# Optimization experiments

Measured on AMD Instinct MI355X. Metric: run time of the kernel, lower is better.

Reference implementation:

```python
import jax, jax.numpy as jnp
import numpy as np

TAU = 2.0
V_TH = 1.0
SG_ALPHA = 4.0  # spikingjelly surrogate.Sigmoid default

@jax.custom_vjp
def spike_fn(u):
    # heaviside(u) with sigmoid surrogate gradient; u = v - v_threshold
    return (u >= 0.0).astype(u.dtype)

def _spike_fwd(u):
    return spike_fn(u), u

def _spike_bwd(u, g):
    s = jax.nn.sigmoid(SG_ALPHA * u)
    return (g * SG_ALPHA * s * (1.0 - s),)

spike_fn.defvjp(_spike_fwd, _spike_bwd)

def lif_scan(h):
    # h: [T, B, D] input currents; multi-step LIF with hard reset to 0,
    # decay_input=True: v = v + (h - v) / tau
    def step(v, h_t):
        v = v + (h_t - v) / TAU
        s = spike_fn(v - V_TH)
        v = v * (1.0 - jax.lax.stop_gradient(s))  # detach_reset=True, v_reset=0
        return v, s
    v0 = jnp.zeros_like(h[0])
    _, spikes = jax.lax.scan(step, v0, h)
    return spikes  # [T, B, D]

def setup_inputs() -> dict:
    key = jax.random.key(0)
    k_x, k_w1, k_b1, k_w2, k_b2 = jax.random.split(key, 5)
    T, B, D, C = 32, 512, 1024, 1000
    lim1 = 1.0 / np.sqrt(D)
    return {
        "x": jax.random.normal(k_x, (T, B, D), dtype=jnp.float32),
        "W1": jax.random.uniform(k_w1, (D, D), jnp.float32, -lim1, lim1),
        "b1": jax.random.uniform(k_b1, (D,), jnp.float32, -lim1, lim1),
        "W2": jax.random.uniform(k_w2, (C, D), jnp.float32, -lim1, lim1),
        "b2": jax.random.uniform(k_b2, (C,), jnp.float32, -lim1, lim1),
    }

def reference(x, W1, b1, W2, b2):
    # linear_1: [T,B,D] @ [D,D]^T + b1
    h = jnp.einsum('tbd,ed->tbe', x, W1) + b1
    s = lif_scan(h)                               # [T,B,D] spikes in {0,1}
    y = jnp.einsum('tbd,cd->tbc', s, W2) + b2     # [T,B,C]
    y = y.mean(axis=0)                            # [B,C]
    return jax.nn.log_softmax(y, axis=1)
```

## Files before the change

kernel.cpp:

```cpp
#include <hip/hip_runtime.h>
#include <math.h>

#define T_STEPS 32
#define B_SZ    512
#define D_SZ    1024
#define C_SZ    1000
#define KZ      8
#define HP      132

typedef __bf16 bf16x8 __attribute__((ext_vector_type(8)));
typedef float  f32x4  __attribute__((ext_vector_type(4)));

__device__ __forceinline__ unsigned short f2bf(float f) {
    unsigned u = __float_as_uint(f);
    unsigned r = u + 0x7FFFu + ((u >> 16) & 1u);
    return (unsigned short)(r >> 16);
}
__device__ __forceinline__ float bf2f(unsigned short b) {
    return __uint_as_float(((unsigned)b) << 16);
}

__device__ __forceinline__ void async_copy16(const void* g, void* l) {
    __builtin_amdgcn_global_load_lds(
        (const __attribute__((address_space(1))) unsigned int*)g,
        (__attribute__((address_space(3))) unsigned int*)l,
        16, 0, 0);
}

__device__ __forceinline__ bf16x8 cvt8(const float4 u, const float4 v) {
    bf16x8 r;
    r[0] = (__bf16)u.x; r[1] = (__bf16)u.y; r[2] = (__bf16)u.z; r[3] = (__bf16)u.w;
    r[4] = (__bf16)v.x; r[5] = (__bf16)v.y; r[6] = (__bf16)v.z; r[7] = (__bf16)v.w;
    return r;
}

#define NW14  262144
#define NW24  256000
#define NWTOT (NW14 + NW24)

__global__ __launch_bounds__(256) void cast_w_k(
    const float* __restrict__ W1, unsigned short* __restrict__ W1_bf,
    const float* __restrict__ W2, unsigned short* __restrict__ W2_bf)
{
    const int idx = blockIdx.x * 256 + threadIdx.x;
    const float4* s; ushort4* d; int j;
    if (idx < NW14) { s = (const float4*)W1; d = (ushort4*)W1_bf; j = idx; }
    else            { s = (const float4*)W2; d = (ushort4*)W2_bf; j = idx - NW14; }
    const float4 v = s[j];
    ushort4 o;
    o.x = f2bf(v.x); o.y = f2bf(v.y); o.z = f2bf(v.z); o.w = f2bf(v.w);
    d[j] = o;
}

__global__ __launch_bounds__(256) void gemm1_scan_k(
    const float* __restrict__ X, const unsigned short* __restrict__ Bm,
    const float* __restrict__ bias, unsigned short* __restrict__ cnt)
{
    __shared__ __align__(16) unsigned short smem[128 * HP];
    unsigned short* As = smem;
    unsigned short* Bs = smem + 8192;

    const int tid  = threadIdx.x;
    const int wave = tid >> 6;
    const int lane = tid & 63;
    const int lm   = lane & 15;
    const int quad = lane >> 4;
    const int wm   = (wave >> 1) * 64;
    const int wn   = (wave & 1) * 64;

    const int f  = blockIdx.x;
    const int yb = f & 127;
    const int xb = f >> 7;
    const int b0 = yb * 4;
    const int n0 = xb * 128;

    f32x4 acc[4][4];
    #pragma unroll
    for (int i = 0; i < 4; ++i)
        #pragma unroll
        for (int j = 0; j < 4; ++j)
            acc[i][j] = (f32x4){0.f, 0.f, 0.f, 0.f};

    int srow[4], sgq[4];
    size_t arowoff[4];
    unsigned ldsoffB[4];
    #pragma unroll
    for (int p = 0; p < 4; ++p) {
        const int s = p * 256 + tid;
        const int rho = s >> 3;
        srow[p] = rho;
        sgq[p]  = (s & 7) ^ (rho & 7);
        arowoff[p] = (size_t)((rho >> 2) * 512 + b0 + (rho & 3)) * D_SZ;
        ldsoffB[p] = (unsigned)(p * 256 + wave * 64) * 16u;
    }
    const int fq0 = quad ^ (lm & 7);

    for (int k0 = 0; k0 < D_SZ; k0 += 64) {
        #pragma unroll
        for (int p = 0; p < 4; ++p)
            async_copy16(Bm + (size_t)(n0 + srow[p]) * D_SZ + k0 + sgq[p] * 8,
                         (char*)Bs + ldsoffB[p]);
        #pragma unroll
        for (int p = 0; p < 4; ++p) {
            const float* src = X + arowoff[p] + k0 + sgq[p] * 8;
            const float4 u = *(const float4*)(src);
            const float4 v = *(const float4*)(src + 4);
            ((bf16x8*)As)[p * 256 + tid] = cvt8(u, v);
        }
        __syncthreads();

        #pragma unroll
        for (int kk = 0; kk < 2; ++kk) {
            const int fqk = fq0 ^ (kk * 4);
            bf16x8 af[4], bfr[4];
            #pragma unroll
            for (int i = 0; i < 4; ++i) {
                af[i]  = ((const bf16x8*)As)[(wm + i * 16 + lm) * 8 + fqk];
                bfr[i] = ((const bf16x8*)Bs)[(wn + i * 16 + lm) * 8 + fqk];
            }
            #pragma unroll
            for (int mi = 0; mi < 4; ++mi)
                #pragma unroll
                for (int ni = 0; ni < 4; ++ni)
                    acc[mi][ni] = __builtin_amdgcn_mfma_f32_16x16x32_bf16(
                        af[mi], bfr[ni], acc[mi][ni], 0, 0, 0);
        }
        __syncthreads();
    }

    #pragma unroll
    for (int ni = 0; ni < 4; ++ni) {
        const int nn = wn + ni * 16 + lm;
        const float bv = bias[n0 + nn];
        #pragma unroll
        for (int mi = 0; mi < 4; ++mi) {
            const f32x4 v = acc[mi][ni];
            #pragma unroll
            for (int r = 0; r < 4; ++r)
                smem[(wm + mi * 16 + quad * 4 + r) * HP + nn] = f2bf(v[r] + bv);
        }
    }
    __syncthreads();

    {
        const unsigned* smemU = (const unsigned*)smem;
        const int bb = tid >> 6;
        const int c2 = tid & 63;
        float v0 = 0.f, cv0 = 0.f, v1 = 0.f, cv1 = 0.f;
        #pragma unroll
        for (int t = 0; t < T_STEPS; ++t) {
            const unsigned u = smemU[(t * 4 + bb) * (HP / 2) + c2];
            const float h0 = bf2f((unsigned short)(u & 0xFFFFu));
            const float h1 = bf2f((unsigned short)(u >> 16));
            v0 = 0.5f * (v0 + h0);
            const float s0 = (v0 >= 1.0f) ? 1.0f : 0.0f;
            cv0 += s0; v0 *= (1.0f - s0);
            v1 = 0.5f * (v1 + h1);
            const float s1 = (v1 >= 1.0f) ? 1.0f : 0.0f;
            cv1 += s1; v1 *= (1.0f - s1);
        }
        ushort2 o;
        o.x = f2bf(cv0); o.y = f2bf(cv1);
        *(ushort2*)&cnt[(size_t)(b0 + bb) * D_SZ + n0 + 2 * c2] = o;
    }
}

__global__ __launch_bounds__(256) void gemm2_splitk_k(
    const unsigned short* __restrict__ A, const unsigned short* __restrict__ Bm,
    float* __restrict__ partial)
{
    __shared__ __align__(16) unsigned short As[128 * 32];
    __shared__ __align__(16) unsigned short Bs[128 * 32];

    const int tid  = threadIdx.x;
    const int wave = tid >> 6;
    const int lane = tid & 63;
    const int lm   = lane & 15;
    const int quad = lane >> 4;
    const int wm   = (wave >> 1) * 64;
    const int wn   = (wave & 1) * 64;
    const int n0   = blockIdx.x * 128;
    const int m0   = blockIdx.y * 128;
    const int kz   = blockIdx.z;

    f32x4 acc[4][4];
    #pragma unroll
    for (int i = 0; i < 4; ++i)
        #pragma unroll
        for (int j = 0; j < 4; ++j)
            acc[i][j] = (f32x4){0.f, 0.f, 0.f, 0.f};

    int srow[2], sgq[2];
    unsigned ldsoff[2];
    #pragma unroll
    for (int p = 0; p < 2; ++p) {
        const int s = p * 256 + tid;
        srow[p] = s >> 2;
        sgq[p]  = (s & 3) ^ ((srow[p] >> 1) & 3);
        ldsoff[p] = (unsigned)(p * 256 + wave * 64) * 16u;
    }
    const int fq = quad ^ ((lm >> 1) & 3);

    const int kbeg = kz * (D_SZ / KZ);
    for (int k0 = kbeg; k0 < kbeg + D_SZ / KZ; k0 += 32) {
        #pragma unroll
        for (int p = 0; p < 2; ++p) {
            async_copy16(A + (size_t)(m0 + srow[p]) * D_SZ + k0 + sgq[p] * 8,
                         (char*)As + ldsoff[p]);
            int brow = n0 + srow[p];
            if (brow > C_SZ - 1) brow = C_SZ - 1;
            async_copy16(Bm + (size_t)brow * D_SZ + k0 + sgq[p] * 8,
                         (char*)Bs + ldsoff[p]);
        }
        __syncthreads();

        bf16x8 af[4], bfr[4];
        #pragma unroll
        for (int i = 0; i < 4; ++i) {
            af[i]  = ((const bf16x8*)As)[(wm + i * 16 + lm) * 4 + fq];
            bfr[i] = ((const bf16x8*)Bs)[(wn + i * 16 + lm) * 4 + fq];
        }
        #pragma unroll
        for (int mi = 0; mi < 4; ++mi)
            #pragma unroll
            for (int ni = 0; ni < 4; ++ni)
                acc[mi][ni] = __builtin_amdgcn_mfma_f32_16x16x32_bf16(
                    af[mi], bfr[ni], acc[mi][ni], 0, 0, 0);
        __syncthreads();
    }

    #pragma unroll
    for (int ni = 0; ni < 4; ++ni) {
        const int nn = n0 + wn + ni * 16 + lm;
        if (nn >= C_SZ) continue;
        #pragma unroll
        for (int mi = 0; mi < 4; ++mi) {
            const f32x4 v = acc[mi][ni];
            #pragma unroll
            for (int r = 0; r < 4; ++r) {
                const int mm = m0 + wm + mi * 16 + quad * 4 + r;
                partial[((size_t)kz * B_SZ + mm) * C_SZ + nn] = v[r];
            }
        }
    }
}

__global__ __launch_bounds__(256) void reduce_lsm_k(
    const float* __restrict__ partial, const float* __restrict__ b2,
    float* __restrict__ out)
{
    __shared__ float red_max[4];
    __shared__ float red_sum[4];

    const int b   = blockIdx.x;
    const int tid = threadIdx.x;

    float vals[4];
    float m = -1e30f;
    #pragma unroll
    for (int k = 0; k < 4; ++k) {
        const int c = tid + k * 256;
        if (c < C_SZ) {
            float s = 0.f;
            #pragma unroll
            for (int z = 0; z < KZ; ++z)
                s += partial[((size_t)z * B_SZ + b) * C_SZ + c];
            vals[k] = s * (1.0f / (float)T_STEPS) + b2[c];
        } else {
            vals[k] = -1e30f;
        }
        m = fmaxf(m, vals[k]);
    }
    #pragma unroll
    for (int off = 32; off > 0; off >>= 1)
        m = fmaxf(m, __shfl_down(m, off, 64));
    const int wave = tid >> 6;
    const int lane = tid & 63;
    if (lane == 0) red_max[wave] = m;
    __syncthreads();
    m = fmaxf(fmaxf(red_max[0], red_max[1]), fmaxf(red_max[2], red_max[3]));

    float s = 0.f;
    #pragma unroll
    for (int k = 0; k < 4; ++k) {
        const int c = tid + k * 256;
        if (c < C_SZ) s += __expf(vals[k] - m);
    }
    #pragma unroll
    for (int off = 32; off > 0; off >>= 1)
        s += __shfl_down(s, off, 64);
    if (lane == 0) red_sum[wave] = s;
    __syncthreads();
    s = red_sum[0] + red_sum[1] + red_sum[2] + red_sum[3];

    const float lse = m + logf(s);
    #pragma unroll
    for (int k = 0; k < 4; ++k) {
        const int c = tid + k * 256;
        if (c < C_SZ) out[(size_t)b * C_SZ + c] = vals[k] - lse;
    }
}

extern "C" void kernel_launch(void* const* d_in, const int* in_sizes, int n_in,
                              void* d_out, int out_size, void* d_ws, size_t ws_size,
                              hipStream_t stream)
{
    const float* x  = (const float*)d_in[0];
    const float* W1 = (const float*)d_in[1];
    const float* b1 = (const float*)d_in[2];
    const float* W2 = (const float*)d_in[3];
    const float* b2 = (const float*)d_in[4];
    float* out = (float*)d_out;

    char* ws = (char*)d_ws;
    unsigned short* W1_bf   = (unsigned short*)(ws);
    unsigned short* W2_bf   = (unsigned short*)(ws + 2097152);
    unsigned short* cnt_bf  = (unsigned short*)(ws + 4145152);
    float*          partial = (float*)(ws + 5193728);

    cast_w_k<<<NWTOT / 256, 256, 0, stream>>>(W1, W1_bf, W2, W2_bf);

    gemm1_scan_k<<<(B_SZ / 4) * (D_SZ / 128), 256, 0, stream>>>(
        x, W1_bf, b1, cnt_bf);

    {
        dim3 grid((C_SZ + 127) / 128, B_SZ / 128, KZ);
        gemm2_splitk_k<<<grid, 256, 0, stream>>>(cnt_bf, W2_bf, partial);
    }

    reduce_lsm_k<<<B_SZ, 256, 0, stream>>>(partial, b2, out);
}
```

Measured before the change: 167.5 us.

## Double-buffer GEMM1 LDS tiles with register prefetch and swizzled block order

Converts the GEMM1 main loop into a double-buffered pipeline: the next A tile is prefetched into registers and the next B tile is staged asynchronously into a second LDS buffer while MFMAs run on the current buffer. This drops one barrier per k-step. Compute sections are wrapped in s_setprio so the MFMA waves get issue priority. The block index mapping is also remapped into 8x8 groups for better L2 reuse of X and W1 tiles. In exchange, LDS grows to 64KB and register use rises, which may cut occupancy.

```diff
diff --git a/kernel.cpp b/kernel.cpp
--- a/kernel.cpp
+++ b/kernel.cpp
@@ -56,9 +56,7 @@
     const float* __restrict__ X, const unsigned short* __restrict__ Bm,
     const float* __restrict__ bias, unsigned short* __restrict__ cnt)
 {
-    __shared__ __align__(16) unsigned short smem[128 * HP];
-    unsigned short* As = smem;
-    unsigned short* Bs = smem + 8192;
+    __shared__ __align__(16) unsigned short smem[32768];
 
     const int tid  = threadIdx.x;
     const int wave = tid >> 6;
@@ -69,8 +67,11 @@
     const int wn   = (wave & 1) * 64;
 
     const int f  = blockIdx.x;
-    const int yb = f & 127;
-    const int xb = f >> 7;
+    const int rr = f >> 9;
+    const int cc = f & 7;
+    const int ss = (f >> 3) & 63;
+    const int xb = ss & 7;
+    const int yb = rr * 64 + (ss >> 3) * 8 + cc;
     const int b0 = yb * 4;
     const int n0 = xb * 128;
 
@@ -95,38 +96,85 @@
     }
     const int fq0 = quad ^ (lm & 7);
 
-    for (int k0 = 0; k0 < D_SZ; k0 += 64) {
-        #pragma unroll
-        for (int p = 0; p < 4; ++p)
-            async_copy16(Bm + (size_t)(n0 + srow[p]) * D_SZ + k0 + sgq[p] * 8,
-                         (char*)Bs + ldsoffB[p]);
-        #pragma unroll
-        for (int p = 0; p < 4; ++p) {
-            const float* src = X + arowoff[p] + k0 + sgq[p] * 8;
-            const float4 u = *(const float4*)(src);
-            const float4 v = *(const float4*)(src + 4);
-            ((bf16x8*)As)[p * 256 + tid] = cvt8(u, v);
-        }
+    float4 au[4], av[4];
+
+#define LOAD_A(k0_) do {                                                        \
+        _Pragma("unroll")                                                       \
+        for (int p = 0; p < 4; ++p) {                                           \
+            const float* srcp = X + arowoff[p] + (k0_) + sgq[p] * 8;            \
+            au[p] = *(const float4*)(srcp);                                     \
+            av[p] = *(const float4*)(srcp + 4);                                 \
+        }                                                                       \
+    } while (0)
+
+#define STAGE_B(buf_, k0_) do {                                                 \
+        char* bdst = (char*)(smem + 16384 + (buf_) * 8192);                     \
+        _Pragma("unroll")                                                       \
+        for (int p = 0; p < 4; ++p)                                             \
+            async_copy16(Bm + (size_t)(n0 + srow[p]) * D_SZ + (k0_) + sgq[p] * 8,\
+                         bdst + ldsoffB[p]);                                    \
+    } while (0)
+
+#define WRITE_A(buf_) do {                                                      \
+        bf16x8* adst = (bf16x8*)(smem + (buf_) * 8192);                         \
+        _Pragma("unroll")                                                       \
+        for (int p = 0; p < 4; ++p)                                             \
+            adst[p * 256 + tid] = cvt8(au[p], av[p]);                           \
+    } while (0)
+
+#define COMPUTE(buf_) do {                                                      \
+        const bf16x8* Ar = (const bf16x8*)(smem + (buf_) * 8192);               \
+        const bf16x8* Br = (const bf16x8*)(smem + 16384 + (buf_) * 8192);       \
+        __builtin_amdgcn_s_setprio(1);                                          \
+        _Pragma("unroll")                                                       \
+        for (int kk = 0; kk < 2; ++kk) {                                        \
+            const int fqk = fq0 ^ (kk * 4);                                     \
+            bf16x8 af[4], bfr[4];                                               \
+            _Pragma("unroll")                                                   \
+            for (int i2 = 0; i2 < 4; ++i2) {                                    \
+                af[i2]  = Ar[(wm + i2 * 16 + lm) * 8 + fqk];                    \
+                bfr[i2] = Br[(wn + i2 * 16 + lm) * 8 + fqk];                    \
+            }                                                                   \
+            _Pragma("unroll")                                                   \
+            for (int mi = 0; mi < 4; ++mi)                                      \
+                _Pragma("unroll")                                               \
+                for (int ni = 0; ni < 4; ++ni)                                  \
+                    acc[mi][ni] = __builtin_amdgcn_mfma_f32_16x16x32_bf16(      \
+                        af[mi], bfr[ni], acc[mi][ni], 0, 0, 0);                 \
+        }                                                                       \
+        __builtin_amdgcn_s_setprio(0);                                          \
+    } while (0)
+
+    LOAD_A(0);
+    STAGE_B(0, 0);
+    WRITE_A(0);
+    __syncthreads();
+    LOAD_A(64);
+    STAGE_B(1, 64);
+
+    for (int i = 0; i < 14; i += 2) {
+        COMPUTE(0);
+        WRITE_A(1);
         __syncthreads();
-
-        #pragma unroll
-        for (int kk = 0; kk < 2; ++kk) {
-            const int fqk = fq0 ^ (kk * 4);
-            bf16x8 af[4], bfr[4];
-            #pragma unroll
-            for (int i = 0; i < 4; ++i) {
-                af[i]  = ((const bf16x8*)As)[(wm + i * 16 + lm) * 8 + fqk];
-                bfr[i] = ((const bf16x8*)Bs)[(wn + i * 16 + lm) * 8 + fqk];
-            }
-            #pragma unroll
-            for (int mi = 0; mi < 4; ++mi)
-                #pragma unroll
-                for (int ni = 0; ni < 4; ++ni)
-                    acc[mi][ni] = __builtin_amdgcn_mfma_f32_16x16x32_bf16(
-                        af[mi], bfr[ni], acc[mi][ni], 0, 0, 0);
-        }
+        LOAD_A((i + 2) * 64);
+        STAGE_B(0, (i + 2) * 64);
+
+        COMPUTE(1);
+        WRITE_A(0);
         __syncthreads();
-    }
+        LOAD_A((i + 3) * 64);
+        STAGE_B(1, (i + 3) * 64);
+    }
+    COMPUTE(0);
+    WRITE_A(1);
+    __syncthreads();
+    COMPUTE(1);
+    __syncthreads();
+
+#undef LOAD_A
+#undef STAGE_B
+#undef WRITE_A
+#undef COMPUTE
 
     #pragma unroll
     for (int ni = 0; ni < 4; ++ni) {
```

Result: no change. 168.8 us (+0.8%).

## Rewrite GEMM1+LIF scan kernel with 256x256 tiles and double-buffered LDS pipeline

Applied to the files above, without the earlier changes.

Rewrites the fused GEMM1 and LIF-scan kernel to use 512-thread blocks computing 256x256 output tiles (8 batch rows by 32 timesteps, 256 features) with 128 KB of LDS. A and B tiles are double-buffered so the next k-slice's global loads and async B copies overlap MFMA work. MFMAs are split into phases with barriers and setprio hints. The scan epilogue now uses an XOR-swizzled LDS layout to avoid bank conflicts. Only 256 blocks are launched, so each CU holds one large block, which risks lower occupancy and tail effects in exchange for more data reuse.

```diff
diff --git a/kernel.cpp b/kernel.cpp
--- a/kernel.cpp
+++ b/kernel.cpp
@@ -6,7 +6,6 @@
 #define D_SZ    1024
 #define C_SZ    1000
 #define KZ      8
-#define HP      132
 
 typedef __bf16 bf16x8 __attribute__((ext_vector_type(8)));
 typedef float  f32x4  __attribute__((ext_vector_type(4)));
@@ -52,116 +51,186 @@
     d[j] = o;
 }
 
-__global__ __launch_bounds__(256) void gemm1_scan_k(
-    const float* __restrict__ X, const unsigned short* __restrict__ Bm,
+__global__ __launch_bounds__(512, 2) void gemm1_scan256_k(
+    const float* __restrict__ Xf, const unsigned short* __restrict__ Bm,
     const float* __restrict__ bias, unsigned short* __restrict__ cnt)
 {
-    __shared__ __align__(16) unsigned short smem[128 * HP];
-    unsigned short* As = smem;
-    unsigned short* Bs = smem + 8192;
+    __shared__ __align__(16) unsigned short smem[65536];
 
     const int tid  = threadIdx.x;
     const int wave = tid >> 6;
     const int lane = tid & 63;
     const int lm   = lane & 15;
     const int quad = lane >> 4;
-    const int wm   = (wave >> 1) * 64;
-    const int wn   = (wave & 1) * 64;
-
-    const int f  = blockIdx.x;
-    const int yb = f & 127;
-    const int xb = f >> 7;
-    const int b0 = yb * 4;
-    const int n0 = xb * 128;
-
-    f32x4 acc[4][4];
-    #pragma unroll
-    for (int i = 0; i < 4; ++i)
+    const int wm   = (wave >> 2) * 128;
+    const int wn   = (wave & 3) * 64;
+
+    const int wgid = (blockIdx.x & 7) * 32 + (blockIdx.x >> 3);
+    const int yb = wgid >> 2;
+    const int xb = wgid & 3;
+    const int b0 = yb * 8;
+    const int n0 = xb * 256;
+
+    f32x4 acc[8][4];
+    #pragma unroll
+    for (int i = 0; i < 8; ++i)
         #pragma unroll
         for (int j = 0; j < 4; ++j)
             acc[i][j] = (f32x4){0.f, 0.f, 0.f, 0.f};
 
-    int srow[4], sgq[4];
-    size_t arowoff[4];
-    unsigned ldsoffB[4];
+    unsigned aoff[4], boff[4];
+    unsigned ldsoffp[4];
     #pragma unroll
     for (int p = 0; p < 4; ++p) {
-        const int s = p * 256 + tid;
+        const int s   = p * 512 + tid;
         const int rho = s >> 3;
-        srow[p] = rho;
-        sgq[p]  = (s & 7) ^ (rho & 7);
-        arowoff[p] = (size_t)((rho >> 2) * 512 + b0 + (rho & 3)) * D_SZ;
-        ldsoffB[p] = (unsigned)(p * 256 + wave * 64) * 16u;
+        const int gq  = (s & 7) ^ (rho & 7);
+        aoff[p] = (unsigned)(((rho >> 3) * 512 + b0 + (rho & 7)) * D_SZ + gq * 8);
+        boff[p] = (unsigned)((n0 + rho) * D_SZ + gq * 8);
+        ldsoffp[p] = (unsigned)(p * 512 + wave * 64) * 16u;
     }
     const int fq0 = quad ^ (lm & 7);
 
-    for (int k0 = 0; k0 < D_SZ; k0 += 64) {
-        #pragma unroll
-        for (int p = 0; p < 4; ++p)
-            async_copy16(Bm + (size_t)(n0 + srow[p]) * D_SZ + k0 + sgq[p] * 8,
-                         (char*)Bs + ldsoffB[p]);
-        #pragma unroll
-        for (int p = 0; p < 4; ++p) {
-            const float* src = X + arowoff[p] + k0 + sgq[p] * 8;
-            const float4 u = *(const float4*)(src);
-            const float4 v = *(const float4*)(src + 4);
-            ((bf16x8*)As)[p * 256 + tid] = cvt8(u, v);
-        }
+    float4 au[4], av[4];
+
+#define LOAD_A(k0_) do {                                                         \
+        _Pragma("unroll")                                                        \
+        for (int p = 0; p < 4; ++p) {                                            \
+            const float* sp_ = Xf + aoff[p] + (k0_);                             \
+            au[p] = *(const float4*)(sp_);                                       \
+            av[p] = *(const float4*)(sp_ + 4);                                   \
+        }                                                                        \
+    } while (0)
+
+#define WRITE_A(cb_) do {                                                        \
+        bf16x8* ab_ = (bf16x8*)((char*)smem + (cb_) * 32768);                    \
+        _Pragma("unroll")                                                        \
+        for (int p = 0; p < 4; ++p)                                              \
+            ab_[p * 512 + tid] = cvt8(au[p], av[p]);                             \
+    } while (0)
+
+#define STG_B(cb_, k0_) do {                                                     \
+        char* bb_ = (char*)smem + 65536 + (cb_) * 32768;                         \
+        _Pragma("unroll")                                                        \
+        for (int p = 0; p < 4; ++p)                                              \
+            async_copy16(Bm + boff[p] + (k0_), bb_ + ldsoffp[p]);                \
+    } while (0)
+
+#define READ_A(mi0_) do {                                                        \
+        _Pragma("unroll")                                                        \
+        for (int m2 = 0; m2 < 2; ++m2) {                                         \
+            const int rw_ = wm + ((mi0_) + m2) * 16 + lm;                        \
+            af[m2][0] = Ar[rw_ * 8 + fq0];                                       \
+            af[m2][1] = Ar[rw_ * 8 + (fq0 ^ 4)];                                 \
+        }                                                                        \
+    } while (0)
+
+#define MFMA2(mi0_) do {                                                         \
+        __builtin_amdgcn_s_setprio(1);                                           \
+        _Pragma("unroll")                                                        \
+        for (int kk = 0; kk < 2; ++kk)                                           \
+            _Pragma("unroll")                                                    \
+            for (int m2 = 0; m2 < 2; ++m2)                                       \
+                _Pragma("unroll")                                                \
+                for (int ni = 0; ni < 4; ++ni)                                   \
+                    acc[(mi0_) + m2][ni] = __builtin_amdgcn_mfma_f32_16x16x32_bf16( \
+                        af[m2][kk], bfr[ni][kk], acc[(mi0_) + m2][ni], 0, 0, 0); \
+        __builtin_amdgcn_s_setprio(0);                                           \
+    } while (0)
+
+    LOAD_A(0);
+    STG_B(0, 0);
+    WRITE_A(0);
+    __syncthreads();
+
+    #pragma unroll 2
+    for (int t = 0; t < 16; ++t) {
+        const int c  = t & 1;
+        const bf16x8* Ar = (const bf16x8*)((const char*)smem + c * 32768);
+        const bf16x8* Br = (const bf16x8*)((const char*)smem + 65536 + c * 32768);
+        const int kn = (t + 1) * 64;
+        bf16x8 bfr[4][2], af[2][2];
+
+        #pragma unroll
+        for (int ni = 0; ni < 4; ++ni) {
+            const int rw = (wn + ni * 16 + lm) * 8;
+            bfr[ni][0] = Br[rw + fq0];
+            bfr[ni][1] = Br[rw + (fq0 ^ 4)];
+        }
+        READ_A(0);
+        if (t < 15) {
+            LOAD_A(kn);
+            STG_B(c ^ 1, kn);
+        }
+        __builtin_amdgcn_s_barrier();
+        MFMA2(0);
+        __builtin_amdgcn_s_barrier();
+
+        READ_A(2);
+        __builtin_amdgcn_s_barrier();
+        MFMA2(2);
+        __builtin_amdgcn_s_barrier();
+
+        READ_A(4);
+        __builtin_amdgcn_s_barrier();
+        MFMA2(4);
+        __builtin_amdgcn_s_barrier();
+
+        READ_A(6);
+        __builtin_amdgcn_s_barrier();
+        MFMA2(6);
+        if (t < 15) WRITE_A(c ^ 1);
         __syncthreads();
-
-        #pragma unroll
-        for (int kk = 0; kk < 2; ++kk) {
-            const int fqk = fq0 ^ (kk * 4);
-            bf16x8 af[4], bfr[4];
-            #pragma unroll
-            for (int i = 0; i < 4; ++i) {
-                af[i]  = ((const bf16x8*)As)[(wm + i * 16 + lm) * 8 + fqk];
-                bfr[i] = ((const bf16x8*)Bs)[(wn + i * 16 + lm) * 8 + fqk];
-            }
-            #pragma unroll
-            for (int mi = 0; mi < 4; ++mi)
-                #pragma unroll
-                for (int ni = 0; ni < 4; ++ni)
-                    acc[mi][ni] = __builtin_amdgcn_mfma_f32_16x16x32_bf16(
-                        af[mi], bfr[ni], acc[mi][ni], 0, 0, 0);
-        }
-        __syncthreads();
-    }
+    }
+
+#undef LOAD_A
+#undef WRITE_A
+#undef STG_B
+#undef READ_A
+#undef MFMA2
 
     #pragma unroll
     for (int ni = 0; ni < 4; ++ni) {
-        const int nn = wn + ni * 16 + lm;
-        const float bv = bias[n0 + nn];
-        #pragma unroll
-        for (int mi = 0; mi < 4; ++mi) {
+        const int col = wn + ni * 16 + lm;
+        const float bv = bias[n0 + col];
+        #pragma unroll
+        for (int mi = 0; mi < 8; ++mi) {
             const f32x4 v = acc[mi][ni];
             #pragma unroll
-            for (int r = 0; r < 4; ++r)
-                smem[(wm + mi * 16 + quad * 4 + r) * HP + nn] = f2bf(v[r] + bv);
+            for (int q = 0; q < 4; ++q) {
+                const int row = wm + mi * 16 + quad * 4 + q;
+                smem[row * 256 + (col ^ (((row >> 2) & 3) << 4))] = f2bf(v[q] + bv);
+            }
         }
     }
     __syncthreads();
 
     {
         const unsigned* smemU = (const unsigned*)smem;
-        const int bb = tid >> 6;
-        const int c2 = tid & 63;
-        float v0 = 0.f, cv0 = 0.f, v1 = 0.f, cv1 = 0.f;
-        #pragma unroll
-        for (int t = 0; t < T_STEPS; ++t) {
-            const unsigned u = smemU[(t * 4 + bb) * (HP / 2) + c2];
-            const float h0 = bf2f((unsigned short)(u & 0xFFFFu));
-            const float h1 = bf2f((unsigned short)(u >> 16));
-            v0 = 0.5f * (v0 + h0);
-            const float s0 = (v0 >= 1.0f) ? 1.0f : 0.0f;
-            cv0 += s0; v0 *= (1.0f - s0);
-            v1 = 0.5f * (v1 + h1);
-            const float s1 = (v1 >= 1.0f) ? 1.0f : 0.0f;
-            cv1 += s1; v1 *= (1.0f - s1);
-        }
-        ushort2 o;
-        o.x = f2bf(cv0); o.y = f2bf(cv1);
-        *(ushort2*)&cnt[(size_t)(b0 + bb) * D_SZ + n0 + 2 * c2] = o;
+        const int uc = tid & 127;
+        const int h4 = tid >> 7;
+        #pragma unroll
+        for (int g = 0; g < 2; ++g) {
+            const int bb = h4 + g * 4;
+            float v0 = 0.f, cv0 = 0.f, v1 = 0.f, cv1 = 0.f;
+            #pragma unroll
+            for (int t2 = 0; t2 < T_STEPS; ++t2) {
+                const int rho = t2 * 8 + bb;
+                const unsigned u =
+                    smemU[rho * 128 + (uc ^ (((rho >> 2) & 3) << 3))];
+                const float h0 = bf2f((unsigned short)(u & 0xFFFFu));
+                const float h1 = bf2f((unsigned short)(u >> 16));
+                v0 = 0.5f * (v0 + h0);
+                const float s0 = (v0 >= 1.0f) ? 1.0f : 0.0f;
+                cv0 += s0; v0 *= (1.0f - s0);
+                v1 = 0.5f * (v1 + h1);
+                const float s1 = (v1 >= 1.0f) ? 1.0f : 0.0f;
+                cv1 += s1; v1 *= (1.0f - s1);
+            }
+            ushort2 o;
+            o.x = f2bf(cv0); o.y = f2bf(cv1);
+            *(ushort2*)&cnt[(size_t)(b0 + bb) * D_SZ + n0 + 2 * uc] = o;
+        }
     }
 }
 
@@ -237,9 +306,9 @@
         for (int mi = 0; mi < 4; ++mi) {
             const f32x4 v = acc[mi][ni];
             #pragma unroll
-            for (int r = 0; r < 4; ++r) {
-                const int mm = m0 + wm + mi * 16 + quad * 4 + r;
-                partial[((size_t)kz * B_SZ + mm) * C_SZ + nn] = v[r];
+            for (int q = 0; q < 4; ++q) {
+                const int mm = m0 + wm + mi * 16 + quad * 4 + q;
+                partial[((size_t)kz * B_SZ + mm) * C_SZ + nn] = v[q];
             }
         }
     }
@@ -320,8 +389,7 @@
 
     cast_w_k<<<NWTOT / 256, 256, 0, stream>>>(W1, W1_bf, W2, W2_bf);
 
-    gemm1_scan_k<<<(B_SZ / 4) * (D_SZ / 128), 256, 0, stream>>>(
-        x, W1_bf, b1, cnt_bf);
+    gemm1_scan256_k<<<256, 512, 0, stream>>>(x, W1_bf, b1, cnt_bf);
 
     {
         dim3 grid((C_SZ + 127) / 128, B_SZ / 128, KZ);
```

Result: slower. 175.5 us (+4.8%).
